# Kernel tuning notes

Measured on AMD Instinct MI355X. Metric: run time of the kernel, lower is better.

The kernel has to match this reference:

```python
import jax, jax.numpy as jnp
import numpy as np

N = 20000        # nodes
E = 320000       # directed edges (before self-loops)
HEADS = 4
IN_DIM = 256
HID = [256, 128]
ZD = [128, 64]
S = 10           # num_samples in reparameterize
REAL_MIN = 2.2e-10
THETA_MAX = 1000.0
KMIN, KMAX = 0.1, 1000.0
SLOPE = 0.2      # GATConv leaky_relu negative_slope


def setup_inputs() -> dict:
    key = jax.random.key(0)
    ks = jax.random.split(key, 24)
    f32 = jnp.float32
    def p(k, shape, scale):
        return jax.random.normal(k, shape, dtype=f32) * scale
    inp = {}
    inp["x"] = jax.random.normal(ks[0], (N, IN_DIM), dtype=f32)
    inp["edge_index"] = jax.random.randint(ks[1], (2, E), 0, N)
    # layer 0: GAT 256 -> 4 heads x 64 (concat = 256)
    inp["gatW0"] = p(ks[2], (HID[0], IN_DIM), 0.06)
    inp["asrc0"] = p(ks[3], (HEADS, HID[0] // HEADS), 0.1)
    inp["adst0"] = p(ks[4], (HEADS, HID[0] // HEADS), 0.1)
    inp["gatb0"] = p(ks[5], (HID[0],), 0.02)
    inp["fcW0"] = p(ks[6], (ZD[0], HID[0]), 0.06)
    inp["fcb0"] = p(ks[7], (ZD[0],), 0.02)
    inp["shW0"] = p(ks[8], (ZD[0], ZD[0]), 0.08)
    inp["shb0"] = p(ks[9], (ZD[0],), 0.02)
    inp["scW0"] = p(ks[10], (ZD[0], ZD[0]), 0.08)
    inp["scb0"] = p(ks[11], (ZD[0],), 0.02)
    # layer 1: GAT 256 -> 4 heads x 32 (concat = 128)
    inp["gatW1"] = p(ks[12], (HID[1], HID[0]), 0.06)
    inp["asrc1"] = p(ks[13], (HEADS, HID[1] // HEADS), 0.1)
    inp["adst1"] = p(ks[14], (HEADS, HID[1] // HEADS), 0.1)
    inp["gatb1"] = p(ks[15], (HID[1],), 0.02)
    inp["fcW1"] = p(ks[16], (ZD[1], HID[1]), 0.06)
    inp["fcb1"] = p(ks[17], (ZD[1],), 0.02)
    inp["shW1"] = p(ks[18], (ZD[1], ZD[1]), 0.08)
    inp["shb1"] = p(ks[19], (ZD[1],), 0.02)
    inp["scW1"] = p(ks[20], (ZD[1], ZD[1]), 0.08)
    inp["scb1"] = p(ks[21], (ZD[1],), 0.02)
    # Weibull reparameterization noise eps ~ U(0,1), shape (S, z_dim, N)
    inp["eps0"] = jax.random.uniform(ks[22], (S, ZD[0], N), dtype=f32)
    inp["eps1"] = jax.random.uniform(ks[23], (S, ZD[1], N), dtype=f32)
    return inp


def _gat(x, src, dst, W, a_src, a_dst, b):
    """PyG GATConv (shared lin, concat heads, add_self_loops done by caller)."""
    n = x.shape[0]
    xw = (x @ W.T).reshape(n, HEADS, -1)            # [N, H, C]
    s = (xw * a_src[None]).sum(-1)                  # [N, H] alpha_src
    d = (xw * a_dst[None]).sum(-1)                  # [N, H] alpha_dst
    e = s[src] + d[dst]                             # [E, H]
    e = jnp.where(e > 0, e, SLOPE * e)              # leaky_relu
    m = jax.lax.stop_gradient(jax.ops.segment_max(e, dst, num_segments=n))
    ex = jnp.exp(e - m[dst])
    den = jax.ops.segment_sum(ex, dst, num_segments=n)
    alpha = ex / (den[dst] + 1e-16)                 # segment softmax over in-edges
    out = jax.ops.segment_sum(alpha[:, :, None] * xw[src], dst, num_segments=n)
    return out.reshape(n, -1) + b                   # [N, H*C]


def _reparam(k, l, eps):
    # theta = l * (-log(max(1-eps, real_min)))^(1/k), mean over samples, clamp
    lm = jnp.log(jnp.maximum(1.0 - eps, REAL_MIN))  # [S, z, N]
    theta = l[None] * jnp.power(-lm, 1.0 / k[None])
    return jnp.clip(theta.mean(0), REAL_MIN, THETA_MAX)


def _right(h, Wk, bk, Wl, bl, eps):
    k = jnp.clip(jax.nn.softplus(h @ Wk.T + bk).T, KMIN, KMAX)      # [z, N]
    l = jnp.maximum(jax.nn.softplus(h @ Wl.T + bl).T, REAL_MIN)     # [z, N]
    l = l / jnp.exp(jax.lax.lgamma(1.0 + 1.0 / k))
    return _reparam(k, l, eps), k, l


def reference(x, edge_index, gatW0, asrc0, adst0, gatb0, fcW0, fcb0, shW0, shb0,
              scW0, scb0, gatW1, asrc1, adst1, gatb1, fcW1, fcb1, shW1, shb1,
              scW1, scb1, eps0, eps1):
    n = x.shape[0]
    loops = jnp.arange(n)
    src = jnp.concatenate([edge_index[0], loops])   # GATConv add_self_loops
    dst = jnp.concatenate([edge_index[1], loops])
    h0 = _gat(x, src, dst, gatW0, asrc0, adst0, gatb0)
    z0 = jax.nn.softplus(h0 @ fcW0.T + fcb0)
    h1 = _gat(h0, src, dst, gatW1, asrc1, adst1, gatb1)
    z1 = jax.nn.softplus(h1 @ fcW1.T + fcb1)
    theta1, k1, l1 = _right(z1, shW1, shb1, scW1, scb1, eps1)
    theta0, k0, l0 = _right(z0, shW0, shb0, scW0, scb0, eps0)
    return (theta0, theta1, k0, k1, l0, l1)
```

## Files before the change

### kernel.cpp

```cpp
#include <hip/hip_runtime.h>
#include <math.h>

#define N_NODES 20000
#define E_EDGES 320000
#define NHEADS 4
#define RMIN 2.2e-10f
#define THETA_MAX 1000.0f
#define SLOPE 0.2f

__device__ __forceinline__ float softplus_f(float x) {
    return fmaxf(x, 0.0f) + log1pf(expf(-fabsf(x)));
}

__global__ __launch_bounds__(256) void count_kernel(const int* __restrict__ dst,
                                                    int* __restrict__ deg) {
    int e = blockIdx.x * 256 + threadIdx.x;
    if (e < E_EDGES) atomicAdd(&deg[dst[e]], 1);
}

__global__ __launch_bounds__(256) void scan_kernel(const int* __restrict__ deg,
                                                   int* __restrict__ rowptr,
                                                   int* __restrict__ cursor) {
    __shared__ int part[256];
    int t = threadIdx.x;
    const int CH = (N_NODES + 255) / 256;
    int base = t * CH;
    int sum = 0;
    for (int i = 0; i < CH; ++i) {
        int idx = base + i;
        if (idx < N_NODES) sum += deg[idx];
    }
    part[t] = sum;
    __syncthreads();
    for (int off = 1; off < 256; off <<= 1) {
        int v = (t >= off) ? part[t - off] : 0;
        __syncthreads();
        part[t] += v;
        __syncthreads();
    }
    int run = (t == 0) ? 0 : part[t - 1];
    for (int i = 0; i < CH; ++i) {
        int idx = base + i;
        if (idx < N_NODES) {
            rowptr[idx] = run;
            cursor[idx] = run;
            run += deg[idx];
        }
    }
    if (t == 255) rowptr[N_NODES] = run;
}

__global__ __launch_bounds__(256) void scatter_kernel(const int* __restrict__ src,
                                                      const int* __restrict__ dst,
                                                      int* __restrict__ cursor,
                                                      int* __restrict__ csr,
                                                      int* __restrict__ dnd) {
    int e = blockIdx.x * 256 + threadIdx.x;
    if (e < E_EDGES) {
        int dn = dst[e];
        int p = atomicAdd(&cursor[dn], 1);
        csr[p] = src[e];
        dnd[p] = dn;
    }
}

__global__ __launch_bounds__(256) void eweight_kernel(const int* __restrict__ csr,
                                                      const int* __restrict__ dnd,
                                                      const float* __restrict__ s,
                                                      const float* __restrict__ d,
                                                      float* __restrict__ w4,
                                                      float* __restrict__ wself) {
    int p = blockIdx.x * 256 + threadIdx.x;
    if (p >= E_EDGES + N_NODES) return;
    int sn, dn;
    float* outp;
    if (p < E_EDGES) {
        sn = csr[p];
        dn = dnd[p];
        outp = w4 + 4 * (size_t)p;
    } else {
        sn = p - E_EDGES;
        dn = sn;
        outp = wself + 4 * (size_t)sn;
    }
    float4 sv = *(const float4*)(s + 4 * (size_t)sn);
    float4 dv = *(const float4*)(d + 4 * (size_t)dn);
    float4 wv;
    float e;
    e = sv.x + dv.x; e = e > 0.f ? e : SLOPE * e; wv.x = expf(e);
    e = sv.y + dv.y; e = e > 0.f ? e : SLOPE * e; wv.y = expf(e);
    e = sv.z + dv.z; e = e > 0.f ? e : SLOPE * e; wv.z = expf(e);
    e = sv.w + dv.w; e = e > 0.f ? e : SLOPE * e; wv.w = expf(e);
    *(float4*)outp = wv;
}

template <int MODE, bool TRANS>
__device__ __forceinline__ void gemm_epilogue4(const float acc[4][4],
                                               const float* __restrict__ bp,
                                               float* __restrict__ op,
                                               int ow, int colbase, int r0, int lc, int M) {
    float bv[4] = {0.f, 0.f, 0.f, 0.f};
    if (MODE != 0) *(float4*)bv = *(const float4*)(bp + colbase + lc);
    float vals[4][4];
#pragma unroll
    for (int i = 0; i < 4; ++i)
#pragma unroll
        for (int j = 0; j < 4; ++j) {
            float v = acc[i][j];
            if (MODE == 1) v = softplus_f(v + bv[j]);
            else if (MODE == 2) { v = softplus_f(v + bv[j]); v = fminf(fmaxf(v, 0.1f), 1000.0f); }
            else if (MODE == 3) { v = fmaxf(softplus_f(v + bv[j]), RMIN); }
            vals[i][j] = v;
        }
    if (!TRANS) {
#pragma unroll
        for (int i = 0; i < 4; ++i) {
            int row = r0 + i;
            if (row < M) *(float4*)(op + (size_t)row * ow + colbase + lc) = *(float4*)vals[i];
        }
    } else {
        if (r0 + 3 < M) {
#pragma unroll
            for (int j = 0; j < 4; ++j) {
                int c = colbase + lc + j;
                float col[4] = {vals[0][j], vals[1][j], vals[2][j], vals[3][j]};
                *(float4*)(op + (size_t)c * M + r0) = *(float4*)col;
            }
        } else {
#pragma unroll
            for (int i = 0; i < 4; ++i) {
                int row = r0 + i;
                if (row < M)
#pragma unroll
                    for (int j = 0; j < 4; ++j) op[(size_t)(colbase + lc + j) * M + row] = vals[i][j];
            }
        }
    }
}

template <int MODE0, int MODE1, bool TRANS>
__global__ __launch_bounds__(256) void gemm64_kernel(const float* __restrict__ A,
                                                     const float* __restrict__ W0,
                                                     const float* __restrict__ W1,
                                                     const float* __restrict__ b0p,
                                                     const float* __restrict__ b1p,
                                                     float* __restrict__ out0,
                                                     float* __restrict__ out1,
                                                     int M, int K, int split, int no1) {
    __shared__ float As[16][68];
    __shared__ float Bs[16][68];
    int tid = threadIdx.x;
    int tx = tid & 15, ty = tid >> 4;
    int bm = blockIdx.x * 64;
    int bn = blockIdx.y * 64;
    bool first = bn < split;
    const float* W = first ? (W0 + (size_t)bn * K) : (W1 + (size_t)(bn - split) * K);
    int m = tid >> 2;
    int kk0 = (tid & 3) * 4;
    int arow = bm + m;
    bool avalid = arow < M;
    const float* Ap = A + (size_t)arow * K + kk0;
    const float* Wp = W + (size_t)m * K + kk0;

    float4 av = make_float4(0.f, 0.f, 0.f, 0.f);
    if (avalid) av = *(const float4*)(Ap);
    float4 bv = *(const float4*)(Wp);

    float acc[4][4] = {};
    int T = K >> 4;
    for (int t = 0; t < T; ++t) {
        As[kk0 + 0][m] = av.x; As[kk0 + 1][m] = av.y;
        As[kk0 + 2][m] = av.z; As[kk0 + 3][m] = av.w;
        Bs[kk0 + 0][m] = bv.x; Bs[kk0 + 1][m] = bv.y;
        Bs[kk0 + 2][m] = bv.z; Bs[kk0 + 3][m] = bv.w;
        __syncthreads();
        if (t + 1 < T) {
            int ko = (t + 1) << 4;
            if (avalid) av = *(const float4*)(Ap + ko);
            bv = *(const float4*)(Wp + ko);
        }
#pragma unroll
        for (int kk = 0; kk < 16; ++kk) {
            float a[4], b[4];
            *(float4*)a = *(const float4*)(&As[kk][ty * 4]);
            *(float4*)b = *(const float4*)(&Bs[kk][tx * 4]);
#pragma unroll
            for (int i = 0; i < 4; ++i)
#pragma unroll
                for (int j = 0; j < 4; ++j) acc[i][j] += a[i] * b[j];
        }
        __syncthreads();
    }
    int r0 = bm + ty * 4;
    int lc = tx * 4;
    if (first) gemm_epilogue4<MODE0, TRANS>(acc, b0p, out0, split, bn, r0, lc, M);
    else       gemm_epilogue4<MODE1, TRANS>(acc, b1p, out1, no1, bn - split, r0, lc, M);
}

template <int F, int CPER>
__global__ __launch_bounds__(256) void sd_kernel(const float* __restrict__ xw,
                                                 const float* __restrict__ asrc,
                                                 const float* __restrict__ adst,
                                                 float* __restrict__ s,
                                                 float* __restrict__ d) {
    int wave = threadIdx.x >> 6;
    int lane = threadIdx.x & 63;
    int n = blockIdx.x * 4 + wave;
    if (n >= N_NODES) return;
    float ss[NHEADS] = {0, 0, 0, 0}, dd[NHEADS] = {0, 0, 0, 0};
#pragma unroll
    for (int j = 0; j < F / 64; ++j) {
        int c = j * 64 + lane;
        int h = c / CPER;
        int cc = c % CPER;
        float v = xw[(size_t)n * F + c];
        ss[h] += v * asrc[h * CPER + cc];
        dd[h] += v * adst[h * CPER + cc];
    }
#pragma unroll
    for (int off = 32; off > 0; off >>= 1) {
#pragma unroll
        for (int h = 0; h < NHEADS; ++h) {
            ss[h] += __shfl_xor(ss[h], off, 64);
            dd[h] += __shfl_xor(dd[h], off, 64);
        }
    }
    if (lane == 0) {
#pragma unroll
        for (int h = 0; h < NHEADS; ++h) {
            s[n * NHEADS + h] = ss[h];
            d[n * NHEADS + h] = dd[h];
        }
    }
}

template <int CPER>
__device__ __forceinline__ float pick_w(float4 w, int j, int lane) {
    if constexpr (CPER == 64) {
        return j == 0 ? w.x : (j == 1 ? w.y : (j == 2 ? w.z : w.w));
    } else {
        float lo = (j == 0) ? w.x : w.z;
        float hi = (j == 0) ? w.y : w.w;
        return (lane & 32) ? hi : lo;
    }
}

template <int F, int CPER>
__global__ __launch_bounds__(256) void agg_kernel(const float* __restrict__ xw,
                                                  const int* __restrict__ rowptr,
                                                  const int* __restrict__ csr,
                                                  const float* __restrict__ w4,
                                                  const float* __restrict__ wself,
                                                  const float* __restrict__ bias,
                                                  float* __restrict__ out) {
    int wave = threadIdx.x >> 6;
    int lane = threadIdx.x & 63;
    int n = blockIdx.x * 4 + wave;
    if (n >= N_NODES) return;
    constexpr int J = F / 64;

    float4 wl = *(const float4*)(wself + 4 * (size_t)n);
    float den[NHEADS] = {wl.x, wl.y, wl.z, wl.w};
    float acc[J];
#pragma unroll
    for (int j = 0; j < J; ++j) {
        int c = j * 64 + lane;
        acc[j] = pick_w<CPER>(wl, j, lane) * xw[(size_t)n * F + c];
    }

    int beg = rowptr[n], end = rowptr[n + 1];
    int idx = beg;
    for (; idx + 2 <= end; idx += 2) {
        int sa = csr[idx], sb = csr[idx + 1];
        float4 wa = *(const float4*)(w4 + 4 * (size_t)idx);
        float4 wb = *(const float4*)(w4 + 4 * (size_t)(idx + 1));
        den[0] += wa.x + wb.x;
        den[1] += wa.y + wb.y;
        den[2] += wa.z + wb.z;
        den[3] += wa.w + wb.w;
        const float* ra = xw + (size_t)sa * F;
        const float* rb = xw + (size_t)sb * F;
#pragma unroll
        for (int j = 0; j < J; ++j) {
            int c = j * 64 + lane;
            acc[j] += pick_w<CPER>(wa, j, lane) * ra[c];
            acc[j] += pick_w<CPER>(wb, j, lane) * rb[c];
        }
    }
    if (idx < end) {
        int sa = csr[idx];
        float4 wa = *(const float4*)(w4 + 4 * (size_t)idx);
        den[0] += wa.x;
        den[1] += wa.y;
        den[2] += wa.z;
        den[3] += wa.w;
        const float* ra = xw + (size_t)sa * F;
#pragma unroll
        for (int j = 0; j < J; ++j) {
            int c = j * 64 + lane;
            acc[j] += pick_w<CPER>(wa, j, lane) * ra[c];
        }
    }

#pragma unroll
    for (int j = 0; j < J; ++j) {
        int c = j * 64 + lane;
        float dv;
        if constexpr (CPER == 64) dv = den[j];
        else dv = (lane & 32) ? den[2 * j + 1] : den[2 * j];
        out[(size_t)n * F + c] = acc[j] / (dv + 1e-16f) + bias[c];
    }
}

__global__ __launch_bounds__(256) void theta_kernel(const float* __restrict__ eps,
                                                    const float* __restrict__ kptr,
                                                    float* __restrict__ lptr,
                                                    float* __restrict__ theta, int ZN) {
    int i = blockIdx.x * 256 + threadIdx.x;
    if (i >= ZN) return;
    float k = kptr[i];
    float invk = 1.0f / k;
    float lg = expf(lgammaf(1.0f + invk));
    float l = lptr[i] / lg;
    lptr[i] = l;
    float acc = 0.0f;
#pragma unroll
    for (int ss = 0; ss < 10; ++ss) {
        float u = eps[(size_t)ss * ZN + i];
        float v = -logf(fmaxf(1.0f - u, RMIN));
        acc += exp2f(log2f(v) * invk);
    }
    float th = l * acc * 0.1f;
    th = fminf(fmaxf(th, RMIN), THETA_MAX);
    theta[i] = th;
}

extern "C" void kernel_launch(void* const* d_in, const int* in_sizes, int n_in,
                              void* d_out, int out_size, void* d_ws, size_t ws_size,
                              hipStream_t stream) {
    const float* x     = (const float*)d_in[0];
    const int*   eidx  = (const int*)d_in[1];
    const float* gatW0 = (const float*)d_in[2];
    const float* asrc0 = (const float*)d_in[3];
    const float* adst0 = (const float*)d_in[4];
    const float* gatb0 = (const float*)d_in[5];
    const float* fcW0  = (const float*)d_in[6];
    const float* fcb0  = (const float*)d_in[7];
    const float* shW0  = (const float*)d_in[8];
    const float* shb0  = (const float*)d_in[9];
    const float* scW0  = (const float*)d_in[10];
    const float* scb0  = (const float*)d_in[11];
    const float* gatW1 = (const float*)d_in[12];
    const float* asrc1 = (const float*)d_in[13];
    const float* adst1 = (const float*)d_in[14];
    const float* gatb1 = (const float*)d_in[15];
    const float* fcW1  = (const float*)d_in[16];
    const float* fcb1  = (const float*)d_in[17];
    const float* shW1  = (const float*)d_in[18];
    const float* shb1  = (const float*)d_in[19];
    const float* scW1  = (const float*)d_in[20];
    const float* scb1  = (const float*)d_in[21];
    const float* eps0  = (const float*)d_in[22];
    const float* eps1  = (const float*)d_in[23];

    const int* e_src = eidx;
    const int* e_dst = eidx + E_EDGES;

    size_t off = 0;
    auto carve = [&](size_t elems) {
        void* p = (char*)d_ws + off;
        off += ((elems * 4 + 255) / 256) * 256;
        return p;
    };
    float* xw0 = (float*)carve(20000u * 256);
    float* h0  = (float*)carve(20000u * 256);
    float* z0  = (float*)carve(20000u * 128);
    float* xw1 = (float*)carve(20000u * 128);
    float* h1  = (float*)carve(20000u * 128);
    float* z1  = (float*)carve(20000u * 64);
    float* s0  = (float*)carve(20000u * 4);
    float* d0  = (float*)carve(20000u * 4);
    float* s1  = (float*)carve(20000u * 4);
    float* d1  = (float*)carve(20000u * 4);
    int* deg    = (int*)carve(20000);
    int* rowptr = (int*)carve(20001);
    int* cursor = (int*)carve(20000);
    int* csr    = (int*)carve(E_EDGES);
    int* dnd    = (int*)carve(E_EDGES);
    float* w4    = (float*)carve((size_t)E_EDGES * 4);
    float* wself = (float*)carve(20000u * 4);

    float* out    = (float*)d_out;
    float* theta0 = out;
    float* theta1 = out + 2560000;
    float* k0     = out + 3840000;
    float* k1     = out + 6400000;
    float* l0     = out + 7680000;
    float* l1     = out + 10240000;

    const int M = N_NODES;
    dim3 blk(256);
    const int GX = (N_NODES + 63) / 64;
    const int EW_BLOCKS = (E_EDGES + N_NODES + 255) / 256;

    (void)hipMemsetAsync(deg, 0, N_NODES * sizeof(int), stream);
    count_kernel<<<(E_EDGES + 255) / 256, blk, 0, stream>>>(e_dst, deg);
    scan_kernel<<<1, blk, 0, stream>>>(deg, rowptr, cursor);
    scatter_kernel<<<(E_EDGES + 255) / 256, blk, 0, stream>>>(e_src, e_dst, cursor, csr, dnd);

    gemm64_kernel<0, 0, false><<<dim3(GX, 4), blk, 0, stream>>>(
        x, gatW0, nullptr, nullptr, nullptr, xw0, nullptr, M, 256, 256, 0);
    sd_kernel<256, 64><<<5000, blk, 0, stream>>>(xw0, asrc0, adst0, s0, d0);
    eweight_kernel<<<EW_BLOCKS, blk, 0, stream>>>(csr, dnd, s0, d0, w4, wself);
    agg_kernel<256, 64><<<5000, blk, 0, stream>>>(xw0, rowptr, csr, w4, wself, gatb0, h0);

    gemm64_kernel<1, 0, false><<<dim3(GX, 4), blk, 0, stream>>>(
        h0, fcW0, gatW1, fcb0, nullptr, z0, xw1, M, 256, 128, 128);

    sd_kernel<128, 32><<<5000, blk, 0, stream>>>(xw1, asrc1, adst1, s1, d1);
    eweight_kernel<<<EW_BLOCKS, blk, 0, stream>>>(csr, dnd, s1, d1, w4, wself);
    agg_kernel<128, 32><<<5000, blk, 0, stream>>>(xw1, rowptr, csr, w4, wself, gatb1, h1);
    gemm64_kernel<1, 0, false><<<dim3(GX, 1), blk, 0, stream>>>(
        h1, fcW1, nullptr, fcb1, nullptr, z1, nullptr, M, 128, 64, 0);

    gemm64_kernel<2, 3, true><<<dim3(GX, 4), blk, 0, stream>>>(
        z0, shW0, scW0, shb0, scb0, k0, l0, M, 128, 128, 128);
    gemm64_kernel<2, 3, true><<<dim3(GX, 2), blk, 0, stream>>>(
        z1, shW1, scW1, shb1, scb1, k1, l1, M, 64, 64, 64);

    theta_kernel<<<(2560000 + 255) / 256, blk, 0, stream>>>(eps0, k0, l0, theta0, 2560000);
    theta_kernel<<<(1280000 + 255) / 256, blk, 0, stream>>>(eps1, k1, l1, theta1, 1280000);
}
```

Baseline: 626.3 us.

## Fuse attention scores into GEMM epilogue and edge weights into aggregation

Computes the per-head alpha_src/alpha_dst dot products inside the GEMM epilogue with wave shuffles, which removes the separate sd_kernel passes. Edge attention weights are now recomputed on the fly in the aggregation kernel instead of being materialized by eweight_kernel, so the w4/wself/dnd buffers and their memory traffic go away. The fc1 GEMM is merged with the layer-0 shape/scale GEMMs into one launch, and the two theta launches become one. The cost is redundant expf work per edge inside the aggregation loop and an extra gather of s per neighbor.

```diff
diff --git a/kernel.cpp b/kernel.cpp
--- a/kernel.cpp
+++ b/kernel.cpp
@@ -10,6 +10,16 @@
 
 __device__ __forceinline__ float softplus_f(float x) {
     return fmaxf(x, 0.0f) + log1pf(expf(-fabsf(x)));
+}
+
+__device__ __forceinline__ float4 edge_w(float4 sv, float4 dv) {
+    float4 w;
+    float e;
+    e = sv.x + dv.x; e = e > 0.f ? e : SLOPE * e; w.x = expf(e);
+    e = sv.y + dv.y; e = e > 0.f ? e : SLOPE * e; w.y = expf(e);
+    e = sv.z + dv.z; e = e > 0.f ? e : SLOPE * e; w.z = expf(e);
+    e = sv.w + dv.w; e = e > 0.f ? e : SLOPE * e; w.w = expf(e);
+    return w;
 }
 
 __global__ __launch_bounds__(256) void count_kernel(const int* __restrict__ dst,
@@ -53,45 +63,12 @@
 __global__ __launch_bounds__(256) void scatter_kernel(const int* __restrict__ src,
                                                       const int* __restrict__ dst,
                                                       int* __restrict__ cursor,
-                                                      int* __restrict__ csr,
-                                                      int* __restrict__ dnd) {
+                                                      int* __restrict__ csr) {
     int e = blockIdx.x * 256 + threadIdx.x;
     if (e < E_EDGES) {
-        int dn = dst[e];
-        int p = atomicAdd(&cursor[dn], 1);
+        int p = atomicAdd(&cursor[dst[e]], 1);
         csr[p] = src[e];
-        dnd[p] = dn;
-    }
-}
-
-__global__ __launch_bounds__(256) void eweight_kernel(const int* __restrict__ csr,
-                                                      const int* __restrict__ dnd,
-                                                      const float* __restrict__ s,
-                                                      const float* __restrict__ d,
-                                                      float* __restrict__ w4,
-                                                      float* __restrict__ wself) {
-    int p = blockIdx.x * 256 + threadIdx.x;
-    if (p >= E_EDGES + N_NODES) return;
-    int sn, dn;
-    float* outp;
-    if (p < E_EDGES) {
-        sn = csr[p];
-        dn = dnd[p];
-        outp = w4 + 4 * (size_t)p;
-    } else {
-        sn = p - E_EDGES;
-        dn = sn;
-        outp = wself + 4 * (size_t)sn;
-    }
-    float4 sv = *(const float4*)(s + 4 * (size_t)sn);
-    float4 dv = *(const float4*)(d + 4 * (size_t)dn);
-    float4 wv;
-    float e;
-    e = sv.x + dv.x; e = e > 0.f ? e : SLOPE * e; wv.x = expf(e);
-    e = sv.y + dv.y; e = e > 0.f ? e : SLOPE * e; wv.y = expf(e);
-    e = sv.z + dv.z; e = e > 0.f ? e : SLOPE * e; wv.z = expf(e);
-    e = sv.w + dv.w; e = e > 0.f ? e : SLOPE * e; wv.w = expf(e);
-    *(float4*)outp = wv;
+    }
 }
 
 template <int MODE, bool TRANS>
@@ -138,7 +115,7 @@
     }
 }
 
-template <int MODE0, int MODE1, bool TRANS>
+template <int MODE0, int MODE1, bool TRANS, int SDW, int CPER>
 __global__ __launch_bounds__(256) void gemm64_kernel(const float* __restrict__ A,
                                                      const float* __restrict__ W0,
                                                      const float* __restrict__ W1,
@@ -146,6 +123,10 @@
                                                      const float* __restrict__ b1p,
                                                      float* __restrict__ out0,
                                                      float* __restrict__ out1,
+                                                     const float* __restrict__ asrc,
+                                                     const float* __restrict__ adst,
+                                                     float* __restrict__ sp,
+                                                     float* __restrict__ dp,
                                                      int M, int K, int split, int no1) {
     __shared__ float As[16][68];
     __shared__ float Bs[16][68];
@@ -193,45 +174,113 @@
     }
     int r0 = bm + ty * 4;
     int lc = tx * 4;
+
+    if constexpr (SDW != 0) {
+        bool dosd = (SDW == 1) ? first : !first;
+        if (dosd) {
+            int bo = (SDW == 1) ? bn : bn - split;
+            float4 as4 = *(const float4*)(asrc + bo + lc);
+            float4 ad4 = *(const float4*)(adst + bo + lc);
+            float ps[4], pd[4];
+#pragma unroll
+            for (int i = 0; i < 4; ++i) {
+                ps[i] = acc[i][0] * as4.x + acc[i][1] * as4.y + acc[i][2] * as4.z + acc[i][3] * as4.w;
+                pd[i] = acc[i][0] * ad4.x + acc[i][1] * ad4.y + acc[i][2] * ad4.z + acc[i][3] * ad4.w;
+            }
+#pragma unroll
+            for (int off = (CPER == 64 ? 8 : 4); off >= 1; off >>= 1) {
+#pragma unroll
+                for (int i = 0; i < 4; ++i) {
+                    ps[i] += __shfl_xor(ps[i], off, 64);
+                    pd[i] += __shfl_xor(pd[i], off, 64);
+                }
+            }
+            bool lanesel;
+            int h;
+            if constexpr (CPER == 64) { lanesel = (tx == 0); h = bo >> 6; }
+            else { lanesel = ((tx & 7) == 0); h = (bo >> 5) + (tx >> 3); }
+            if (lanesel) {
+#pragma unroll
+                for (int i = 0; i < 4; ++i) {
+                    int row = r0 + i;
+                    if (row < M) {
+                        sp[row * NHEADS + h] = ps[i];
+                        dp[row * NHEADS + h] = pd[i];
+                    }
+                }
+            }
+        }
+    }
+
     if (first) gemm_epilogue4<MODE0, TRANS>(acc, b0p, out0, split, bn, r0, lc, M);
     else       gemm_epilogue4<MODE1, TRANS>(acc, b1p, out1, no1, bn - split, r0, lc, M);
 }
 
-template <int F, int CPER>
-__global__ __launch_bounds__(256) void sd_kernel(const float* __restrict__ xw,
-                                                 const float* __restrict__ asrc,
-                                                 const float* __restrict__ adst,
-                                                 float* __restrict__ s,
-                                                 float* __restrict__ d) {
-    int wave = threadIdx.x >> 6;
-    int lane = threadIdx.x & 63;
-    int n = blockIdx.x * 4 + wave;
-    if (n >= N_NODES) return;
-    float ss[NHEADS] = {0, 0, 0, 0}, dd[NHEADS] = {0, 0, 0, 0};
-#pragma unroll
-    for (int j = 0; j < F / 64; ++j) {
-        int c = j * 64 + lane;
-        int h = c / CPER;
-        int cc = c % CPER;
-        float v = xw[(size_t)n * F + c];
-        ss[h] += v * asrc[h * CPER + cc];
-        dd[h] += v * adst[h * CPER + cc];
-    }
-#pragma unroll
-    for (int off = 32; off > 0; off >>= 1) {
-#pragma unroll
-        for (int h = 0; h < NHEADS; ++h) {
-            ss[h] += __shfl_xor(ss[h], off, 64);
-            dd[h] += __shfl_xor(dd[h], off, 64);
-        }
-    }
-    if (lane == 0) {
-#pragma unroll
-        for (int h = 0; h < NHEADS; ++h) {
-            s[n * NHEADS + h] = ss[h];
-            d[n * NHEADS + h] = dd[h];
-        }
-    }
+__global__ __launch_bounds__(256) void gemmC_kernel(const float* __restrict__ h1,
+                                                    const float* __restrict__ fcW1,
+                                                    const float* __restrict__ fcb1,
+                                                    float* __restrict__ z1,
+                                                    const float* __restrict__ z0,
+                                                    const float* __restrict__ shW0,
+                                                    const float* __restrict__ shb0,
+                                                    float* __restrict__ k0,
+                                                    const float* __restrict__ scW0,
+                                                    const float* __restrict__ scb0,
+                                                    float* __restrict__ l0,
+                                                    int M) {
+    constexpr int K = 128;
+    __shared__ float As[16][68];
+    __shared__ float Bs[16][68];
+    int tid = threadIdx.x;
+    int tx = tid & 15, ty = tid >> 4;
+    int bm = blockIdx.x * 64;
+    int y = blockIdx.y;
+    const float* A;
+    const float* W;
+    if (y == 0)      { A = h1; W = fcW1; }
+    else if (y <= 2) { A = z0; W = shW0 + (size_t)(y - 1) * 64 * K; }
+    else             { A = z0; W = scW0 + (size_t)(y - 3) * 64 * K; }
+    int m = tid >> 2;
+    int kk0 = (tid & 3) * 4;
+    int arow = bm + m;
+    bool avalid = arow < M;
+    const float* Ap = A + (size_t)arow * K + kk0;
+    const float* Wp = W + (size_t)m * K + kk0;
+
+    float4 av = make_float4(0.f, 0.f, 0.f, 0.f);
+    if (avalid) av = *(const float4*)(Ap);
+    float4 bv = *(const float4*)(Wp);
+
+    float acc[4][4] = {};
+    constexpr int T = K >> 4;
+    for (int t = 0; t < T; ++t) {
+        As[kk0 + 0][m] = av.x; As[kk0 + 1][m] = av.y;
+        As[kk0 + 2][m] = av.z; As[kk0 + 3][m] = av.w;
+        Bs[kk0 + 0][m] = bv.x; Bs[kk0 + 1][m] = bv.y;
+        Bs[kk0 + 2][m] = bv.z; Bs[kk0 + 3][m] = bv.w;
+        __syncthreads();
+        if (t + 1 < T) {
+            int ko = (t + 1) << 4;
+            if (avalid) av = *(const float4*)(Ap + ko);
+            bv = *(const float4*)(Wp + ko);
+        }
+#pragma unroll
+        for (int kk = 0; kk < 16; ++kk) {
+            float a[4], b[4];
+            *(float4*)a = *(const float4*)(&As[kk][ty * 4]);
+            *(float4*)b = *(const float4*)(&Bs[kk][tx * 4]);
+#pragma unroll
+            for (int i = 0; i < 4; ++i)
+#pragma unroll
+                for (int j = 0; j < 4; ++j) acc[i][j] += a[i] * b[j];
+        }
+        __syncthreads();
+    }
+    int r0 = bm + ty * 4;
+    int lc = tx * 4;
+    if (y == 0)      gemm_epilogue4<1, false>(acc, fcb1, z1, 64, 0, r0, lc, M);
+    else if (y <= 2) gemm_epilogue4<2, true>(acc, shb0, k0, 128, (y - 1) * 64, r0, lc, M);
+    else             gemm_epilogue4<3, true>(acc, scb0, l0, 128, (y - 3) * 64, r0, lc, M);
 }
 
 template <int CPER>
@@ -249,8 +298,8 @@
 __global__ __launch_bounds__(256) void agg_kernel(const float* __restrict__ xw,
                                                   const int* __restrict__ rowptr,
                                                   const int* __restrict__ csr,
-                                                  const float* __restrict__ w4,
-                                                  const float* __restrict__ wself,
+                                                  const float* __restrict__ s,
+                                                  const float* __restrict__ d,
                                                   const float* __restrict__ bias,
                                                   float* __restrict__ out) {
     int wave = threadIdx.x >> 6;
@@ -259,7 +308,9 @@
     if (n >= N_NODES) return;
     constexpr int J = F / 64;
 
-    float4 wl = *(const float4*)(wself + 4 * (size_t)n);
+    float4 d4 = *(const float4*)(d + 4 * (size_t)n);
+    float4 s4 = *(const float4*)(s + 4 * (size_t)n);
+    float4 wl = edge_w(s4, d4);
     float den[NHEADS] = {wl.x, wl.y, wl.z, wl.w};
     float acc[J];
 #pragma unroll
@@ -272,8 +323,8 @@
     int idx = beg;
     for (; idx + 2 <= end; idx += 2) {
         int sa = csr[idx], sb = csr[idx + 1];
-        float4 wa = *(const float4*)(w4 + 4 * (size_t)idx);
-        float4 wb = *(const float4*)(w4 + 4 * (size_t)(idx + 1));
+        float4 wa = edge_w(*(const float4*)(s + 4 * (size_t)sa), d4);
+        float4 wb = edge_w(*(const float4*)(s + 4 * (size_t)sb), d4);
         den[0] += wa.x + wb.x;
         den[1] += wa.y + wb.y;
         den[2] += wa.z + wb.z;
@@ -289,7 +340,7 @@
     }
     if (idx < end) {
         int sa = csr[idx];
-        float4 wa = *(const float4*)(w4 + 4 * (size_t)idx);
+        float4 wa = edge_w(*(const float4*)(s + 4 * (size_t)sa), d4);
         den[0] += wa.x;
         den[1] += wa.y;
         den[2] += wa.z;
@@ -312,12 +363,10 @@
     }
 }
 
-__global__ __launch_bounds__(256) void theta_kernel(const float* __restrict__ eps,
-                                                    const float* __restrict__ kptr,
-                                                    float* __restrict__ lptr,
-                                                    float* __restrict__ theta, int ZN) {
-    int i = blockIdx.x * 256 + threadIdx.x;
-    if (i >= ZN) return;
+__device__ __forceinline__ void theta_work(const float* __restrict__ eps,
+                                           const float* __restrict__ kptr,
+                                           float* __restrict__ lptr,
+                                           float* __restrict__ theta, int i, int ZN) {
     float k = kptr[i];
     float invk = 1.0f / k;
     float lg = expf(lgammaf(1.0f + invk));
@@ -333,6 +382,23 @@
     float th = l * acc * 0.1f;
     th = fminf(fmaxf(th, RMIN), THETA_MAX);
     theta[i] = th;
+}
+
+__global__ __launch_bounds__(256) void theta2_kernel(const float* __restrict__ eps0,
+                                                     float* __restrict__ k0,
+                                                     float* __restrict__ l0,
+                                                     float* __restrict__ th0,
+                                                     const float* __restrict__ eps1,
+                                                     float* __restrict__ k1,
+                                                     float* __restrict__ l1,
+                                                     float* __restrict__ th1) {
+    int i = blockIdx.x * 256 + threadIdx.x;
+    if (i < 2560000) {
+        theta_work(eps0, k0, l0, th0, i, 2560000);
+    } else {
+        int j = i - 2560000;
+        if (j < 1280000) theta_work(eps1, k1, l1, th1, j, 1280000);
+    }
 }
 
 extern "C" void kernel_launch(void* const* d_in, const int* in_sizes, int n_in,
@@ -386,9 +452,6 @@
     int* rowptr = (int*)carve(20001);
     int* cursor = (int*)carve(20000);
     int* csr    = (int*)carve(E_EDGES);
-    int* dnd    = (int*)carve(E_EDGES);
-    float* w4    = (float*)carve((size_t)E_EDGES * 4);
-    float* wself = (float*)carve(20000u * 4);
 
     float* out    = (float*)d_out;
     float* theta0 = out;
@@ -401,33 +464,28 @@
     const int M = N_NODES;
     dim3 blk(256);
     const int GX = (N_NODES + 63) / 64;
-    const int EW_BLOCKS = (E_EDGES + N_NODES + 255) / 256;
 
     (void)hipMemsetAsync(deg, 0, N_NODES * sizeof(int), stream);
     count_kernel<<<(E_EDGES + 255) / 256, blk, 0, stream>>>(e_dst, deg);
     scan_kernel<<<1, blk, 0, stream>>>(deg, rowptr, cursor);
-    scatter_kernel<<<(E_EDGES + 255) / 256, blk, 0, stream>>>(e_src, e_dst, cursor, csr, dnd);
-
-    gemm64_kernel<0, 0, false><<<dim3(GX, 4), blk, 0, stream>>>(
-        x, gatW0, nullptr, nullptr, nullptr, xw0, nullptr, M, 256, 256, 0);
-    sd_kernel<256, 64><<<5000, blk, 0, stream>>>(xw0, asrc0, adst0, s0, d0);
-    eweight_kernel<<<EW_BLOCKS, blk, 0, stream>>>(csr, dnd, s0, d0, w4, wself);
-    agg_kernel<256, 64><<<5000, blk, 0, stream>>>(xw0, rowptr, csr, w4, wself, gatb0, h0);
-
-    gemm64_kernel<1, 0, false><<<dim3(GX, 4), blk, 0, stream>>>(
-        h0, fcW0, gatW1, fcb0, nullptr, z0, xw1, M, 256, 128, 128);
-
-    sd_kernel<128, 32><<<5000, blk, 0, stream>>>(xw1, asrc1, adst1, s1, d1);
-    eweight_kernel<<<EW_BLOCKS, blk, 0, stream>>>(csr, dnd, s1, d1, w4, wself);
-    agg_kernel<128, 32><<<5000, blk, 0, stream>>>(xw1, rowptr, csr, w4, wself, gatb1, h1);
-    gemm64_kernel<1, 0, false><<<dim3(GX, 1), blk, 0, stream>>>(
-        h1, fcW1, nullptr, fcb1, nullptr, z1, nullptr, M, 128, 64, 0);
-
-    gemm64_kernel<2, 3, true><<<dim3(GX, 4), blk, 0, stream>>>(
-        z0, shW0, scW0, shb0, scb0, k0, l0, M, 128, 128, 128);
-    gemm64_kernel<2, 3, true><<<dim3(GX, 2), blk, 0, stream>>>(
-        z1, shW1, scW1, shb1, scb1, k1, l1, M, 64, 64, 64);
-
-    theta_kernel<<<(2560000 + 255) / 256, blk, 0, stream>>>(eps0, k0, l0, theta0, 2560000);
-    theta_kernel<<<(1280000 + 255) / 256, blk, 0, stream>>>(eps1, k1, l1, theta1, 1280000);
-}
+    scatter_kernel<<<(E_EDGES + 255) / 256, blk, 0, stream>>>(e_src, e_dst, cursor, csr);
+
+    gemm64_kernel<0, 0, false, 1, 64><<<dim3(GX, 4), blk, 0, stream>>>(
+        x, gatW0, nullptr, nullptr, nullptr, xw0, nullptr,
+        asrc0, adst0, s0, d0, M, 256, 256, 0);
+    agg_kernel<256, 64><<<5000, blk, 0, stream>>>(xw0, rowptr, csr, s0, d0, gatb0, h0);
+
+    gemm64_kernel<1, 0, false, 2, 32><<<dim3(GX, 4), blk, 0, stream>>>(
+        h0, fcW0, gatW1, fcb0, nullptr, z0, xw1,
+        asrc1, adst1, s1, d1, M, 256, 128, 128);
+    agg_kernel<128, 32><<<5000, blk, 0, stream>>>(xw1, rowptr, csr, s1, d1, gatb1, h1);
+
+    gemmC_kernel<<<dim3(GX, 5), blk, 0, stream>>>(
+        h1, fcW1, fcb1, z1, z0, shW0, shb0, k0, scW0, scb0, l0, M);
+
+    gemm64_kernel<2, 3, true, 0, 64><<<dim3(GX, 2), blk, 0, stream>>>(
+        z1, shW1, scW1, shb1, scb1, k1, l1,
+        nullptr, nullptr, nullptr, nullptr, M, 64, 64, 64);
+
+    theta2_kernel<<<15000, blk, 0, stream>>>(eps0, k0, l0, theta0, eps1, k1, l1, theta1);
+}
```

New measurement: 620.0 us. About the same (-1.0%).
